# Optimization experiments

Hardware: AMD Instinct MI355X
Metric: run time of the kernel (lower is better)

## Reference

```python
import jax, jax.numpy as jnp
import numpy as np

B, C, CI, H, W = 4, 64, 32, 96, 96  # batch, in_channels, inter_channels, height, width


def conv2d(x, w, b, stride=1, pad=0):
    out = jax.lax.conv_general_dilated(
        x, w, (stride, stride), [(pad, pad), (pad, pad)],
        dimension_numbers=('NCHW', 'OIHW', 'NCHW'))
    return out + b[None, :, None, None]


def maxpool2(x):
    return jax.lax.reduce_window(x, -jnp.inf, jax.lax.max, (1, 1, 2, 2), (1, 1, 2, 2), 'VALID')


def up2(x):
    return jnp.repeat(jnp.repeat(x, 2, axis=2), 2, axis=3)


def bn_train(x, gamma, beta, eps=1e-5):
    # BatchNorm2d in training mode: batch statistics over (N, H, W)
    m = jnp.mean(x, axis=(0, 2, 3), keepdims=True)
    v = jnp.var(x, axis=(0, 2, 3), keepdims=True)
    return gamma[None, :, None, None] * (x - m) * jax.lax.rsqrt(v + eps) + beta[None, :, None, None]


def setup_inputs() -> dict:
    key = jax.random.key(0)
    ks = jax.random.split(key, 20)
    s1 = (2.0 / C) ** 0.5            # kaiming-ish for 1x1 convs
    s3 = (2.0 / (C * 9)) ** 0.5      # kaiming-ish for 3x3 convs
    sw = (2.0 / CI) ** 0.5
    return {
        'x':         jax.random.normal(ks[0], (B, C, H, W), jnp.float32),
        'x_pan':     jax.random.normal(ks[1], (B, C, H, W), jnp.float32),
        'g_w':       jax.random.normal(ks[2], (CI, C, 1, 1), jnp.float32) * s1,
        'g_b':       jnp.zeros((CI,), jnp.float32),
        'g_pan_w':   jax.random.normal(ks[3], (CI, C, 1, 1), jnp.float32) * s1,
        'g_pan_b':   jnp.zeros((CI,), jnp.float32),
        'theta_w':   jax.random.normal(ks[4], (CI, C, 3, 3), jnp.float32) * s3,
        'theta_b':   jax.random.normal(ks[5], (CI,), jnp.float32) * 0.02,
        'phi_w':     jax.random.normal(ks[6], (CI, C, 3, 3), jnp.float32) * s3,
        'phi_b':     jax.random.normal(ks[7], (CI,), jnp.float32) * 0.02,
        'phi_pan_w': jax.random.normal(ks[8], (CI, C, 3, 3), jnp.float32) * s3,
        'phi_pan_b': jax.random.normal(ks[9], (CI,), jnp.float32) * 0.02,
        'W_w':       jax.random.normal(ks[10], (C, CI, 1, 1), jnp.float32) * sw,
        'W_b':       jnp.zeros((C,), jnp.float32),
        'W_gamma':   jnp.ones((C,), jnp.float32),
        'W_beta':    jnp.zeros((C,), jnp.float32),
        'Wp_w':      jax.random.normal(ks[11], (C, CI, 1, 1), jnp.float32) * sw,
        'Wp_b':      jnp.zeros((C,), jnp.float32),
        'Wp_gamma':  jnp.ones((C,), jnp.float32),
        'Wp_beta':   jnp.zeros((C,), jnp.float32),
    }


def reference(x, x_pan, g_w, g_b, g_pan_w, g_pan_b, theta_w, theta_b,
              phi_w, phi_b, phi_pan_w, phi_pan_b,
              W_w, W_b, W_gamma, W_beta, Wp_w, Wp_b, Wp_gamma, Wp_beta):
    b = x.shape[0]
    # self branch
    g_x = maxpool2(conv2d(x, g_w, g_b)).reshape(b, CI, -1)                           # (B,CI,M)
    theta = up2(conv2d(x, theta_w, theta_b, stride=2, pad=1)).reshape(b, CI, -1)     # (B,CI,N)
    phi = up2(maxpool2(conv2d(x, phi_w, phi_b, stride=2, pad=1))).reshape(b, CI, -1) # (B,CI,M)
    f = jnp.einsum('bcn,bcm->bnm', theta, phi)                                       # (B,N,M)
    a = jax.nn.softmax(f, axis=-1)
    y = jnp.einsum('bnm,bcm->bcn', a, g_x).reshape(b, CI, H, W)
    W_y = bn_train(conv2d(y, W_w, W_b), W_gamma, W_beta)
    # cross-modal (pan) branch, sharing theta queries
    g_p = maxpool2(conv2d(x_pan, g_pan_w, g_pan_b)).reshape(b, CI, -1)
    phi_p = up2(maxpool2(conv2d(x_pan, phi_pan_w, phi_pan_b, stride=2, pad=1))).reshape(b, CI, -1)
    f_p = jnp.einsum('bcn,bcm->bnm', theta, phi_p)
    a_p = jax.nn.softmax(f_p, axis=-1)
    y_p = jnp.einsum('bnm,bcm->bcn', a_p, g_p).reshape(b, CI, H, W)
    Wp_y = bn_train(conv2d(y_p, Wp_w, Wp_b), Wp_gamma, Wp_beta)
    return jnp.concatenate([W_y, Wp_y], axis=1)  # (B, 2C, H, W)
```

## Files before the change

### kernel.cpp

```cpp
#include <hip/hip_runtime.h>
#include <math.h>

#define BB   4
#define CIN  64
#define CMID 32
#define HS   96
#define WS   96
#define H2   48
#define W2   48
#define H4   24
#define W4   24
#define N2   (H2*W2)
#define M4   (H4*W4)

__global__ __launch_bounds__(256) void zero_kernel(float* __restrict__ p)
{
    p[threadIdx.x] = 0.f;
}

__global__ __launch_bounds__(128) void conv3x3_kernel(
    const float* __restrict__ x, const float* __restrict__ x_pan,
    const float* __restrict__ theta_w, const float* __restrict__ phi_w,
    const float* __restrict__ phi_pan_w,
    float* __restrict__ Ptheta, float* __restrict__ Pphi)
{
    const int bx = blockIdx.x;
    const int b  = blockIdx.y;
    const int cz = blockIdx.z;

    __shared__ __align__(16) float xs[16][5][104];
    __shared__ float wsm[16][9][32];

    const int tid = threadIdx.x;
    const int c16 = tid & 15;
    const int g   = tid >> 4;

    const float* xin = (cz == 2) ? x_pan : x;
    const float* wgt = (cz == 0) ? theta_w : (cz == 1 ? phi_w : phi_pan_w);

    const int p    = bx >> 1;
    const int half = bx & 1;
    const int row0 = 4*p - 1;

    float acc[2][2][6];
    #pragma unroll
    for (int u = 0; u < 2; ++u)
        #pragma unroll
        for (int o = 0; o < 2; ++o)
            #pragma unroll
            for (int j = 0; j < 6; ++j) acc[u][o][j] = 0.f;

    for (int chunk = 0; chunk < 2; ++chunk) {
        const int ci0 = half*32 + chunk*16;
        __syncthreads();
        for (int u = tid; u < 16*5*26; u += 128) {
            int ci = u / 130, rem = u % 130, rr = rem / 26, k = rem % 26;
            int row = row0 + rr;
            float4 v = {0.f,0.f,0.f,0.f};
            if (row >= 0 && row < HS && k >= 2)
                v = *(const float4*)&xin[((b*CIN + ci0 + ci)*HS + row)*WS + 4*k - 8];
            *(float4*)&xs[ci][rr][4*k] = v;
        }
        for (int u = tid; u < 1152; u += 128) {
            int c2 = u / 36, f = u % 36;
            float4 wv = *(const float4*)&wgt[c2*576 + ci0*9 + 4*f];
            int lin = 4*f;
            wsm[(lin  )/9][(lin  )%9][c2] = wv.x;
            wsm[(lin+1)/9][(lin+1)%9][c2] = wv.y;
            wsm[(lin+2)/9][(lin+2)%9][c2] = wv.z;
            wsm[(lin+3)/9][(lin+3)%9][c2] = wv.w;
        }
        __syncthreads();

        for (int ci = 0; ci < 16; ++ci) {
            float w9a[9], w9b[9];
            #pragma unroll
            for (int kk = 0; kk < 9; ++kk) {
                w9a[kk] = wsm[ci][kk][c16];
                w9b[kk] = wsm[ci][kk][c16 + 16];
            }
            #pragma unroll
            for (int rr = 0; rr < 5; ++rr) {
                const float4* xr = (const float4*)&xs[ci][rr][12*g + 4];
                float4 t0 = xr[0], t1 = xr[1], t2 = xr[2], t3 = xr[3];
                float xv[16] = {t0.x,t0.y,t0.z,t0.w, t1.x,t1.y,t1.z,t1.w,
                                t2.x,t2.y,t2.z,t2.w, t3.x,t3.y,t3.z,t3.w};
                if (rr <= 2) {
                    #pragma unroll
                    for (int j = 0; j < 6; ++j)
                        #pragma unroll
                        for (int kw = 0; kw < 3; ++kw) {
                            float xvv = xv[3 + 2*j + kw];
                            acc[0][0][j] += w9a[rr*3+kw] * xvv;
                            acc[1][0][j] += w9b[rr*3+kw] * xvv;
                        }
                }
                if (rr >= 2) {
                    #pragma unroll
                    for (int j = 0; j < 6; ++j)
                        #pragma unroll
                        for (int kw = 0; kw < 3; ++kw) {
                            float xvv = xv[3 + 2*j + kw];
                            acc[0][1][j] += w9a[(rr-2)*3+kw] * xvv;
                            acc[1][1][j] += w9b[(rr-2)*3+kw] * xvv;
                        }
                }
            }
        }
    }

    if (cz == 0) {
        #pragma unroll
        for (int u = 0; u < 2; ++u)
            #pragma unroll
            for (int o = 0; o < 2; ++o)
                #pragma unroll
                for (int j = 0; j < 6; ++j) {
                    int n = (2*p + o)*48 + 6*g + j;
                    Ptheta[((size_t)(half*4 + b)*N2 + n)*32 + c16 + 16*u] = acc[u][o][j];
                }
    } else {
        const int brn = cz - 1;
        #pragma unroll
        for (int u = 0; u < 2; ++u) {
            float* Pb = Pphi + (size_t)(((half*2 + brn)*4 + b)*32 + c16 + 16*u)*N2;
            #pragma unroll
            for (int o = 0; o < 2; ++o)
                #pragma unroll
                for (int j = 0; j < 6; ++j)
                    Pb[(2*p + o)*48 + 6*g + j] = acc[u][o][j];
        }
    }
}

__global__ __launch_bounds__(256) void phipool_kernel(
    const float* __restrict__ Pphi,
    const float* __restrict__ phi_b, const float* __restrict__ phi_pan_b,
    float* __restrict__ Kp)
{
    const int o = blockIdx.x*256 + threadIdx.x;
    const int br   = o / 73728;
    const int rem  = o % 73728;
    const int b    = rem / 18432;
    const int rem2 = rem % 18432;
    const int co   = rem2 / 576;
    const int k    = rem2 % 576;
    const int pr   = k / 24, pc = k % 24;

    const int h1 = 2*4*32*N2;
    const int base = (((br*4 + b)*32 + co)*48 + 2*pr)*48 + 2*pc;
    float2 a0 = *(const float2*)&Pphi[base];
    float2 a1 = *(const float2*)&Pphi[base + 48];
    float2 c0 = *(const float2*)&Pphi[h1 + base];
    float2 c1 = *(const float2*)&Pphi[h1 + base + 48];
    float v00 = a0.x + c0.x, v01 = a0.y + c0.y;
    float v10 = a1.x + c1.x, v11 = a1.y + c1.y;
    float bv = (br ? phi_pan_b : phi_b)[co];
    Kp[((size_t)(br*4 + b)*576 + k)*32 + co] =
        fmaxf(fmaxf(v00, v01), fmaxf(v10, v11)) + bv;
}

__global__ __launch_bounds__(384) void gconv_kernel(
    const float* __restrict__ x, const float* __restrict__ x_pan,
    const float* __restrict__ g_w, const float* __restrict__ g_b,
    const float* __restrict__ g_pan_w, const float* __restrict__ g_pan_b,
    float* __restrict__ Vv)
{
    const int r4 = blockIdx.x;
    const int ch = blockIdx.y;
    const int bb = blockIdx.z;
    const int br = bb >> 2, b = bb & 3;
    const float* xin = br ? x_pan : x;
    const float* wg  = br ? g_pan_w : g_w;

    __shared__ __align__(16) float xs[32][4][48];
    __shared__ float wl[64*33];
    const int tid = threadIdx.x;
    for (int u = tid; u < 2048; u += 384) {
        int c2 = u >> 6, ci = u & 63;
        wl[ci*33 + c2] = wg[u];
    }

    const int c  = tid & 31;
    const int sl = tid >> 5;
    float4 ac0 = {0,0,0,0}, ac1 = {0,0,0,0}, ac2 = {0,0,0,0}, ac3 = {0,0,0,0};

    for (int ci0 = 0; ci0 < 64; ci0 += 32) {
        __syncthreads();
        for (int u = tid; u < 32*4*12; u += 384) {
            int ci = u / 48, rem = u % 48, r = rem / 12, k = rem % 12;
            *(float4*)&xs[ci][r][4*k] =
                *(const float4*)&xin[((b*64 + ci0 + ci)*96 + 4*r4 + r)*96 + ch*48 + 4*k];
        }
        __syncthreads();
        for (int ci = 0; ci < 32; ++ci) {
            const float wv = wl[(ci0 + ci)*33 + c];
            float4 x0 = *(const float4*)&xs[ci][0][4*sl];
            float4 x1 = *(const float4*)&xs[ci][1][4*sl];
            float4 x2 = *(const float4*)&xs[ci][2][4*sl];
            float4 x3 = *(const float4*)&xs[ci][3][4*sl];
            ac0.x += wv*x0.x; ac0.y += wv*x0.y; ac0.z += wv*x0.z; ac0.w += wv*x0.w;
            ac1.x += wv*x1.x; ac1.y += wv*x1.y; ac1.z += wv*x1.z; ac1.w += wv*x1.w;
            ac2.x += wv*x2.x; ac2.y += wv*x2.y; ac2.z += wv*x2.z; ac2.w += wv*x2.w;
            ac3.x += wv*x3.x; ac3.y += wv*x3.y; ac3.z += wv*x3.z; ac3.w += wv*x3.w;
        }
    }
    float m00 = fmaxf(fmaxf(ac0.x, ac0.y), fmaxf(ac1.x, ac1.y));
    float m01 = fmaxf(fmaxf(ac0.z, ac0.w), fmaxf(ac1.z, ac1.w));
    float m10 = fmaxf(fmaxf(ac2.x, ac2.y), fmaxf(ac3.x, ac3.y));
    float m11 = fmaxf(fmaxf(ac2.z, ac2.w), fmaxf(ac3.z, ac3.w));
    float bv = (br ? g_pan_b : g_b)[c];
    const int k = r4*24 + ch*12 + sl;
    Vv[((size_t)bb*576 + k)*32 + c] = 0.25f*(m00+m01+m10+m11) + bv;
}

__global__ __launch_bounds__(256) void attn_kernel(
    const float* __restrict__ Ptheta, const float* __restrict__ theta_b,
    const float* __restrict__ Kp, const float* __restrict__ Vv,
    const float* __restrict__ W_w, const float* __restrict__ W_b,
    const float* __restrict__ Wp_w, const float* __restrict__ Wp_b,
    float* __restrict__ zbuf, float* __restrict__ Psum, float* __restrict__ Psq)
{
    const int qt = blockIdx.x;
    const int bb = blockIdx.y;
    const int b  = bb & 3;
    const int br = bb >> 2;

    __shared__ float Wl[64*33];
    __shared__ float Wb_s[64];
    __shared__ float mbuf[64];
    __shared__ float zsb[64];
    __shared__ float avbuf[64*33];
    __shared__ float ybuf[16*33];

    const int tid  = threadIdx.x;
    const int ql   = tid & 15;
    const int ks   = tid >> 4;
    const int q    = qt*16 + ql;
    const int lane = tid & 63;
    const int w    = tid >> 6;

    const float* Wsrc = br ? Wp_w : W_w;
    for (int u = tid; u < 2048; u += 256)
        Wl[(u >> 5)*33 + (u & 31)] = Wsrc[u];
    if (tid < 64) Wb_s[tid] = (br ? Wp_b : W_b)[tid];

    float qv[32];
    {
        const float4* P0 = (const float4*)(Ptheta + ((size_t)b*N2 + q)*32);
        const float4* P1 = (const float4*)(Ptheta + ((size_t)(4 + b)*N2 + q)*32);
        const float4* TB = (const float4*)theta_b;
        #pragma unroll
        for (int i = 0; i < 8; ++i) {
            float4 a = P0[i], c = P1[i], t = TB[i];
            qv[4*i]   = a.x + c.x + t.x;
            qv[4*i+1] = a.y + c.y + t.y;
            qv[4*i+2] = a.z + c.z + t.z;
            qv[4*i+3] = a.w + c.w + t.w;
        }
    }

    const float* Kb = Kp + (size_t)bb*576*32;
    const float* Vb = Vv + (size_t)bb*576*32;

    float m = -1e30f;
    for (int jj = 0; jj < 9; ++jj) {
        const int k0 = ks*36 + 4*jj;
        float s[4];
        #pragma unroll
        for (int kk = 0; kk < 4; ++kk) {
            const float4* kr = (const float4*)&Kb[(size_t)(k0 + kk)*32];
            float a0 = 0.f, a1 = 0.f;
            #pragma unroll
            for (int c8 = 0; c8 < 8; ++c8) {
                float4 kv = kr[c8];
                a0 += qv[4*c8]*kv.x + qv[4*c8+2]*kv.z;
                a1 += qv[4*c8+1]*kv.y + qv[4*c8+3]*kv.w;
            }
            s[kk] = a0 + a1;
        }
        m = fmaxf(m, fmaxf(fmaxf(s[0], s[1]), fmaxf(s[2], s[3])));
    }
    m = fmaxf(m, __shfl_xor(m, 16));
    m = fmaxf(m, __shfl_xor(m, 32));
    if (lane < 16) mbuf[w*16 + ql] = m;
    __syncthreads();
    const float M = fmaxf(fmaxf(mbuf[ql], mbuf[16+ql]),
                          fmaxf(mbuf[32+ql], mbuf[48+ql]));

    float av[32];
    #pragma unroll
    for (int c2 = 0; c2 < 32; ++c2) av[c2] = 0.f;
    float z = 0.f;
    for (int jj = 0; jj < 9; ++jj) {
        const int k0 = ks*36 + 4*jj;
        float p[4];
        #pragma unroll
        for (int kk = 0; kk < 4; ++kk) {
            const float4* kr = (const float4*)&Kb[(size_t)(k0 + kk)*32];
            float a0 = 0.f, a1 = 0.f;
            #pragma unroll
            for (int c8 = 0; c8 < 8; ++c8) {
                float4 kv = kr[c8];
                a0 += qv[4*c8]*kv.x + qv[4*c8+2]*kv.z;
                a1 += qv[4*c8+1]*kv.y + qv[4*c8+3]*kv.w;
            }
            p[kk] = __expf(a0 + a1 - M);
            z += p[kk];
        }
        #pragma unroll
        for (int kk = 0; kk < 4; ++kk) {
            const float4* vr = (const float4*)&Vb[(size_t)(k0 + kk)*32];
            #pragma unroll
            for (int c8 = 0; c8 < 8; ++c8) {
                float4 vv = vr[c8];
                av[4*c8]   += p[kk]*vv.x;
                av[4*c8+1] += p[kk]*vv.y;
                av[4*c8+2] += p[kk]*vv.z;
                av[4*c8+3] += p[kk]*vv.w;
            }
        }
    }
    z += __shfl_xor(z, 16); z += __shfl_xor(z, 32);
    #pragma unroll
    for (int c2 = 0; c2 < 32; ++c2) {
        av[c2] += __shfl_xor(av[c2], 16);
        av[c2] += __shfl_xor(av[c2], 32);
    }
    if (lane < 16) {
        #pragma unroll
        for (int c2 = 0; c2 < 32; ++c2) avbuf[(w*16 + ql)*33 + c2] = av[c2];
        zsb[w*16 + ql] = z;
    }
    __syncthreads();

    const float Z = zsb[ql] + zsb[16+ql] + zsb[32+ql] + zsb[48+ql];
    const float inv = 1.0f / Z;
    #pragma unroll
    for (int cc = 0; cc < 2; ++cc) {
        const int c2 = 2*ks + cc;
        float sv = avbuf[ql*33 + c2] + avbuf[(16+ql)*33 + c2]
                 + avbuf[(32+ql)*33 + c2] + avbuf[(48+ql)*33 + c2];
        ybuf[ql*33 + c2] = sv * inv;
    }
    __syncthreads();

    #pragma unroll
    for (int i = 0; i < 4; ++i) {
        const int o  = ks*4 + i;
        const int og = br*64 + o;
        float zv = Wb_s[o];
        #pragma unroll
        for (int c2 = 0; c2 < 32; ++c2)
            zv += Wl[o*33 + c2] * ybuf[ql*33 + c2];
        zbuf[((size_t)og*4 + b)*N2 + q] = zv;
        float s1 = zv, s2 = zv*zv;
        #pragma unroll
        for (int d = 1; d < 16; d <<= 1) {
            s1 += __shfl_xor(s1, d);
            s2 += __shfl_xor(s2, d);
        }
        if (ql == 0) {
            atomicAdd(&Psum[og], s1);
            atomicAdd(&Psq[og],  s2);
        }
    }
}

__global__ __launch_bounds__(576) void bnup_kernel(
    const float* __restrict__ zbuf,
    const float* __restrict__ Psum, const float* __restrict__ Psq,
    const float* __restrict__ W_gamma, const float* __restrict__ W_beta,
    const float* __restrict__ Wp_gamma, const float* __restrict__ Wp_beta,
    float* __restrict__ out)
{
    const int og = blockIdx.x, b = blockIdx.y;
    const int br = og >> 6, o = og & 63;
    const float mean = Psum[og] * (1.0f/9216.0f);
    const float var  = Psq[og] * (1.0f/9216.0f) - mean*mean;
    const float gamma = (br ? Wp_gamma : W_gamma)[o];
    const float beta  = (br ? Wp_beta  : W_beta)[o];
    const float scale = gamma * rsqrtf(var + 1e-5f);
    const float shift = beta - mean*scale;

    const int t = threadIdx.x;
    float4 a = *(const float4*)&zbuf[((size_t)og*4 + b)*N2 + 4*t];
    const int r = t / 12, cs = t % 12;
    float v0 = a.x*scale + shift, v1 = a.y*scale + shift;
    float v2 = a.z*scale + shift, v3 = a.w*scale + shift;
    float4 lo = {v0, v0, v1, v1};
    float4 hi = {v2, v2, v3, v3};
    float* ob = out + ((size_t)(b*128 + og)*96 + 2*r)*96 + 8*cs;
    *(float4*)(ob)       = lo;
    *(float4*)(ob + 4)   = hi;
    *(float4*)(ob + 96)  = lo;
    *(float4*)(ob + 100) = hi;
}

extern "C" void kernel_launch(void* const* d_in, const int* in_sizes, int n_in,
                              void* d_out, int out_size, void* d_ws, size_t ws_size,
                              hipStream_t stream) {
    (void)in_sizes; (void)n_in; (void)out_size; (void)ws_size;
    const float* x         = (const float*)d_in[0];
    const float* x_pan     = (const float*)d_in[1];
    const float* g_w       = (const float*)d_in[2];
    const float* g_b       = (const float*)d_in[3];
    const float* g_pan_w   = (const float*)d_in[4];
    const float* g_pan_b   = (const float*)d_in[5];
    const float* theta_w   = (const float*)d_in[6];
    const float* theta_b   = (const float*)d_in[7];
    const float* phi_w     = (const float*)d_in[8];
    const float* phi_b     = (const float*)d_in[9];
    const float* phi_pan_w = (const float*)d_in[10];
    const float* phi_pan_b = (const float*)d_in[11];
    const float* W_w       = (const float*)d_in[12];
    const float* W_b       = (const float*)d_in[13];
    const float* W_gamma   = (const float*)d_in[14];
    const float* W_beta    = (const float*)d_in[15];
    const float* Wp_w      = (const float*)d_in[16];
    const float* Wp_b      = (const float*)d_in[17];
    const float* Wp_gamma  = (const float*)d_in[18];
    const float* Wp_beta   = (const float*)d_in[19];

    float* out = (float*)d_out;
    float* ws  = (float*)d_ws;

    float* Ptheta = ws;
    float* Pphi   = Ptheta + 589824;
    float* zbuf   = Pphi;
    float* Kp     = Pphi + 1179648;
    float* Vv     = Kp + 147456;
    float* Psum   = Vv + 147456;
    float* Psq    = Psum + 128;

    zero_kernel<<<dim3(1), 256, 0, stream>>>(Psum);
    conv3x3_kernel<<<dim3(48, 4, 3), 128, 0, stream>>>(
        x, x_pan, theta_w, phi_w, phi_pan_w, Ptheta, Pphi);
    phipool_kernel<<<dim3(576), 256, 0, stream>>>(Pphi, phi_b, phi_pan_b, Kp);
    gconv_kernel<<<dim3(24, 2, 8), 384, 0, stream>>>(
        x, x_pan, g_w, g_b, g_pan_w, g_pan_b, Vv);
    attn_kernel<<<dim3(144, 8), 256, 0, stream>>>(
        Ptheta, theta_b, Kp, Vv, W_w, W_b, Wp_w, Wp_b, zbuf, Psum, Psq);
    bnup_kernel<<<dim3(128, 4), 576, 0, stream>>>(
        zbuf, Psum, Psq, W_gamma, W_beta, Wp_gamma, Wp_beta, out);
}
```

Measured before the change: 441.1 us.

## Restructure attention to materialize scores in LDS and drop atomic BN stats

The attention kernel now has one thread per key (576 threads). Each thread computes scores for 16 queries and writes them to shared memory, then runs the softmax over those rows and a P·V pass that reads a transposed V layout. This replaces the old two-pass recomputation of QK scores, where each thread also held 32 accumulators. BatchNorm statistics are now written as per-block partial sums and reduced inside bnup, which removes the global atomics and the zero kernel. The conv3x3 channel chunk is halved to shrink LDS use, at the cost of more sync rounds.

```diff
diff --git a/kernel.cpp b/kernel.cpp
--- a/kernel.cpp
+++ b/kernel.cpp
@@ -13,11 +13,6 @@
 #define N2   (H2*W2)
 #define M4   (H4*W4)
 
-__global__ __launch_bounds__(256) void zero_kernel(float* __restrict__ p)
-{
-    p[threadIdx.x] = 0.f;
-}
-
 __global__ __launch_bounds__(128) void conv3x3_kernel(
     const float* __restrict__ x, const float* __restrict__ x_pan,
     const float* __restrict__ theta_w, const float* __restrict__ phi_w,
@@ -28,8 +23,8 @@
     const int b  = blockIdx.y;
     const int cz = blockIdx.z;
 
-    __shared__ __align__(16) float xs[16][5][104];
-    __shared__ float wsm[16][9][32];
+    __shared__ __align__(16) float xs[8][5][104];
+    __shared__ float wsm[8][9][32];
 
     const int tid = threadIdx.x;
     const int c16 = tid & 15;
@@ -50,10 +45,10 @@
             #pragma unroll
             for (int j = 0; j < 6; ++j) acc[u][o][j] = 0.f;
 
-    for (int chunk = 0; chunk < 2; ++chunk) {
-        const int ci0 = half*32 + chunk*16;
+    for (int chunk = 0; chunk < 4; ++chunk) {
+        const int ci0 = half*32 + chunk*8;
         __syncthreads();
-        for (int u = tid; u < 16*5*26; u += 128) {
+        for (int u = tid; u < 8*5*26; u += 128) {
             int ci = u / 130, rem = u % 130, rr = rem / 26, k = rem % 26;
             int row = row0 + rr;
             float4 v = {0.f,0.f,0.f,0.f};
@@ -61,8 +56,8 @@
                 v = *(const float4*)&xin[((b*CIN + ci0 + ci)*HS + row)*WS + 4*k - 8];
             *(float4*)&xs[ci][rr][4*k] = v;
         }
-        for (int u = tid; u < 1152; u += 128) {
-            int c2 = u / 36, f = u % 36;
+        for (int u = tid; u < 576; u += 128) {
+            int c2 = u / 18, f = u % 18;
             float4 wv = *(const float4*)&wgt[c2*576 + ci0*9 + 4*f];
             int lin = 4*f;
             wsm[(lin  )/9][(lin  )%9][c2] = wv.x;
@@ -72,7 +67,7 @@
         }
         __syncthreads();
 
-        for (int ci = 0; ci < 16; ++ci) {
+        for (int ci = 0; ci < 8; ++ci) {
             float w9a[9], w9b[9];
             #pragma unroll
             for (int kk = 0; kk < 9; ++kk) {
@@ -164,7 +159,7 @@
     const float* __restrict__ x, const float* __restrict__ x_pan,
     const float* __restrict__ g_w, const float* __restrict__ g_b,
     const float* __restrict__ g_pan_w, const float* __restrict__ g_pan_b,
-    float* __restrict__ Vv)
+    float* __restrict__ Vt)
 {
     const int r4 = blockIdx.x;
     const int ch = blockIdx.y;
@@ -211,179 +206,181 @@
     float m11 = fmaxf(fmaxf(ac2.z, ac2.w), fmaxf(ac3.z, ac3.w));
     float bv = (br ? g_pan_b : g_b)[c];
     const int k = r4*24 + ch*12 + sl;
-    Vv[((size_t)bb*576 + k)*32 + c] = 0.25f*(m00+m01+m10+m11) + bv;
-}
-
-__global__ __launch_bounds__(256) void attn_kernel(
+    Vt[((size_t)bb*32 + c)*576 + k] = 0.25f*(m00+m01+m10+m11) + bv;
+}
+
+__global__ __launch_bounds__(576, 5) void attn_kernel(
     const float* __restrict__ Ptheta, const float* __restrict__ theta_b,
-    const float* __restrict__ Kp, const float* __restrict__ Vv,
+    const float* __restrict__ Kp, const float* __restrict__ Vt,
     const float* __restrict__ W_w, const float* __restrict__ W_b,
     const float* __restrict__ Wp_w, const float* __restrict__ Wp_b,
-    float* __restrict__ zbuf, float* __restrict__ Psum, float* __restrict__ Psq)
+    float* __restrict__ zbuf, float* __restrict__ Pp1, float* __restrict__ Pp2)
 {
     const int qt = blockIdx.x;
     const int bb = blockIdx.y;
     const int b  = bb & 3;
     const int br = bb >> 2;
-
-    __shared__ float Wl[64*33];
-    __shared__ float Wb_s[64];
-    __shared__ float mbuf[64];
-    __shared__ float zsb[64];
-    __shared__ float avbuf[64*33];
-    __shared__ float ybuf[16*33];
-
-    const int tid  = threadIdx.x;
-    const int ql   = tid & 15;
-    const int ks   = tid >> 4;
-    const int q    = qt*16 + ql;
-    const int lane = tid & 63;
-    const int w    = tid >> 6;
-
+    const int q0 = qt*16;
+
+    __shared__ __align__(16) float Pt[16*580];
+    __shared__ __align__(16) float Qs[16*36];
+    __shared__ float ybuf[16*36];
+    __shared__ float Wt[32*64];
+    __shared__ float zinv[16];
+    __shared__ float s1b[512], s2b[512];
+
+    const int tid = threadIdx.x;
+
+    if (tid < 512) {
+        const int q = tid >> 5, c = tid & 31;
+        Qs[q*36 + c] = Ptheta[((size_t)b*N2 + q0 + q)*32 + c]
+                     + Ptheta[((size_t)(4 + b)*N2 + q0 + q)*32 + c]
+                     + theta_b[c];
+    }
     const float* Wsrc = br ? Wp_w : W_w;
-    for (int u = tid; u < 2048; u += 256)
-        Wl[(u >> 5)*33 + (u & 31)] = Wsrc[u];
-    if (tid < 64) Wb_s[tid] = (br ? Wp_b : W_b)[tid];
-
-    float qv[32];
+    for (int u = tid; u < 2048; u += 576) {
+        const int o = u >> 5, c = u & 31;
+        Wt[c*64 + o] = Wsrc[u];
+    }
+    __syncthreads();
+
     {
-        const float4* P0 = (const float4*)(Ptheta + ((size_t)b*N2 + q)*32);
-        const float4* P1 = (const float4*)(Ptheta + ((size_t)(4 + b)*N2 + q)*32);
-        const float4* TB = (const float4*)theta_b;
-        #pragma unroll
-        for (int i = 0; i < 8; ++i) {
-            float4 a = P0[i], c = P1[i], t = TB[i];
-            qv[4*i]   = a.x + c.x + t.x;
-            qv[4*i+1] = a.y + c.y + t.y;
-            qv[4*i+2] = a.z + c.z + t.z;
-            qv[4*i+3] = a.w + c.w + t.w;
-        }
-    }
-
-    const float* Kb = Kp + (size_t)bb*576*32;
-    const float* Vb = Vv + (size_t)bb*576*32;
-
-    float m = -1e30f;
-    for (int jj = 0; jj < 9; ++jj) {
-        const int k0 = ks*36 + 4*jj;
-        float s[4];
-        #pragma unroll
-        for (int kk = 0; kk < 4; ++kk) {
-            const float4* kr = (const float4*)&Kb[(size_t)(k0 + kk)*32];
-            float a0 = 0.f, a1 = 0.f;
-            #pragma unroll
-            for (int c8 = 0; c8 < 8; ++c8) {
-                float4 kv = kr[c8];
-                a0 += qv[4*c8]*kv.x + qv[4*c8+2]*kv.z;
-                a1 += qv[4*c8+1]*kv.y + qv[4*c8+3]*kv.w;
+        const float* krow = Kp + ((size_t)bb*576 + tid)*32;
+        float4 kf[8];
+        #pragma unroll
+        for (int i = 0; i < 8; ++i) kf[i] = ((const float4*)krow)[i];
+        float s[16];
+        #pragma unroll
+        for (int q = 0; q < 16; ++q) {
+            const float4* qr = (const float4*)&Qs[q*36];
+            float a0 = 0.f, a1 = 0.f, a2 = 0.f, a3 = 0.f;
+            #pragma unroll
+            for (int i = 0; i < 8; ++i) {
+                float4 qf = qr[i];
+                a0 += qf.x*kf[i].x; a1 += qf.y*kf[i].y;
+                a2 += qf.z*kf[i].z; a3 += qf.w*kf[i].w;
             }
-            s[kk] = a0 + a1;
-        }
-        m = fmaxf(m, fmaxf(fmaxf(s[0], s[1]), fmaxf(s[2], s[3])));
-    }
-    m = fmaxf(m, __shfl_xor(m, 16));
-    m = fmaxf(m, __shfl_xor(m, 32));
-    if (lane < 16) mbuf[w*16 + ql] = m;
-    __syncthreads();
-    const float M = fmaxf(fmaxf(mbuf[ql], mbuf[16+ql]),
-                          fmaxf(mbuf[32+ql], mbuf[48+ql]));
-
-    float av[32];
-    #pragma unroll
-    for (int c2 = 0; c2 < 32; ++c2) av[c2] = 0.f;
-    float z = 0.f;
-    for (int jj = 0; jj < 9; ++jj) {
-        const int k0 = ks*36 + 4*jj;
-        float p[4];
-        #pragma unroll
-        for (int kk = 0; kk < 4; ++kk) {
-            const float4* kr = (const float4*)&Kb[(size_t)(k0 + kk)*32];
-            float a0 = 0.f, a1 = 0.f;
-            #pragma unroll
-            for (int c8 = 0; c8 < 8; ++c8) {
-                float4 kv = kr[c8];
-                a0 += qv[4*c8]*kv.x + qv[4*c8+2]*kv.z;
-                a1 += qv[4*c8+1]*kv.y + qv[4*c8+3]*kv.w;
-            }
-            p[kk] = __expf(a0 + a1 - M);
-            z += p[kk];
-        }
-        #pragma unroll
-        for (int kk = 0; kk < 4; ++kk) {
-            const float4* vr = (const float4*)&Vb[(size_t)(k0 + kk)*32];
-            #pragma unroll
-            for (int c8 = 0; c8 < 8; ++c8) {
-                float4 vv = vr[c8];
-                av[4*c8]   += p[kk]*vv.x;
-                av[4*c8+1] += p[kk]*vv.y;
-                av[4*c8+2] += p[kk]*vv.z;
-                av[4*c8+3] += p[kk]*vv.w;
-            }
-        }
-    }
-    z += __shfl_xor(z, 16); z += __shfl_xor(z, 32);
-    #pragma unroll
-    for (int c2 = 0; c2 < 32; ++c2) {
-        av[c2] += __shfl_xor(av[c2], 16);
-        av[c2] += __shfl_xor(av[c2], 32);
-    }
-    if (lane < 16) {
-        #pragma unroll
-        for (int c2 = 0; c2 < 32; ++c2) avbuf[(w*16 + ql)*33 + c2] = av[c2];
-        zsb[w*16 + ql] = z;
-    }
-    __syncthreads();
-
-    const float Z = zsb[ql] + zsb[16+ql] + zsb[32+ql] + zsb[48+ql];
-    const float inv = 1.0f / Z;
-    #pragma unroll
-    for (int cc = 0; cc < 2; ++cc) {
-        const int c2 = 2*ks + cc;
-        float sv = avbuf[ql*33 + c2] + avbuf[(16+ql)*33 + c2]
-                 + avbuf[(32+ql)*33 + c2] + avbuf[(48+ql)*33 + c2];
-        ybuf[ql*33 + c2] = sv * inv;
-    }
-    __syncthreads();
-
-    #pragma unroll
-    for (int i = 0; i < 4; ++i) {
-        const int o  = ks*4 + i;
-        const int og = br*64 + o;
-        float zv = Wb_s[o];
-        #pragma unroll
-        for (int c2 = 0; c2 < 32; ++c2)
-            zv += Wl[o*33 + c2] * ybuf[ql*33 + c2];
-        zbuf[((size_t)og*4 + b)*N2 + q] = zv;
-        float s1 = zv, s2 = zv*zv;
-        #pragma unroll
-        for (int d = 1; d < 16; d <<= 1) {
-            s1 += __shfl_xor(s1, d);
-            s2 += __shfl_xor(s2, d);
-        }
-        if (ql == 0) {
-            atomicAdd(&Psum[og], s1);
-            atomicAdd(&Psq[og],  s2);
-        }
+            s[q] = (a0 + a1) + (a2 + a3);
+        }
+        #pragma unroll
+        for (int q = 0; q < 16; ++q) Pt[q*580 + tid] = s[q];
+    }
+    __syncthreads();
+
+    if (tid < 256) {
+        const int q = tid >> 4, sl = tid & 15;
+        float* row = &Pt[q*580 + 36*sl];
+        float4 f[9];
+        #pragma unroll
+        for (int j = 0; j < 9; ++j) f[j] = *(const float4*)&row[4*j];
+        float m = -1e30f;
+        #pragma unroll
+        for (int j = 0; j < 9; ++j)
+            m = fmaxf(m, fmaxf(fmaxf(f[j].x, f[j].y), fmaxf(f[j].z, f[j].w)));
+        m = fmaxf(m, __shfl_xor(m, 1));
+        m = fmaxf(m, __shfl_xor(m, 2));
+        m = fmaxf(m, __shfl_xor(m, 4));
+        m = fmaxf(m, __shfl_xor(m, 8));
+        float z = 0.f;
+        #pragma unroll
+        for (int j = 0; j < 9; ++j) {
+            f[j].x = __expf(f[j].x - m); f[j].y = __expf(f[j].y - m);
+            f[j].z = __expf(f[j].z - m); f[j].w = __expf(f[j].w - m);
+            z += (f[j].x + f[j].y) + (f[j].z + f[j].w);
+            *(float4*)&row[4*j] = f[j];
+        }
+        z += __shfl_xor(z, 1); z += __shfl_xor(z, 2);
+        z += __shfl_xor(z, 4); z += __shfl_xor(z, 8);
+        if (sl == 0) zinv[q] = 1.0f / z;
+    }
+    __syncthreads();
+
+    if (tid < 512) {
+        const int q = tid >> 5, c = tid & 31;
+        const float* vrow = Vt + ((size_t)bb*32 + c)*576;
+        const float* prow = &Pt[q*580];
+        float a0 = 0.f, a1 = 0.f, a2 = 0.f, a3 = 0.f;
+        #pragma unroll 4
+        for (int kk = 0; kk < 144; ++kk) {
+            float4 pa = *(const float4*)&prow[4*kk];
+            float4 va = *(const float4*)&vrow[4*kk];
+            a0 += pa.x*va.x; a1 += pa.y*va.y;
+            a2 += pa.z*va.z; a3 += pa.w*va.w;
+        }
+        ybuf[q*36 + c] = ((a0 + a1) + (a2 + a3)) * zinv[q];
+    }
+    __syncthreads();
+
+    if (tid < 512) {
+        const int q = tid >> 5, o2 = tid & 31;
+        const float* Wbias = br ? Wp_b : W_b;
+        float z0a = 0.f, z0b = 0.f, z1a = 0.f, z1b = 0.f;
+        #pragma unroll
+        for (int c2 = 0; c2 < 32; c2 += 2) {
+            float y0 = ybuf[q*36 + c2], y1 = ybuf[q*36 + c2 + 1];
+            z0a += Wt[c2*64 + o2]*y0;        z0b += Wt[(c2+1)*64 + o2]*y1;
+            z1a += Wt[c2*64 + o2 + 32]*y0;   z1b += Wt[(c2+1)*64 + o2 + 32]*y1;
+        }
+        float z0 = Wbias[o2]      + z0a + z0b;
+        float z1 = Wbias[o2 + 32] + z1a + z1b;
+        const int n = q0 + q;
+        zbuf[((size_t)(br*64 + o2)*4 + b)*N2 + n]      = z0;
+        zbuf[((size_t)(br*64 + o2 + 32)*4 + b)*N2 + n] = z1;
+        float t0 = z0 + __shfl_xor(z0, 32);
+        float t1 = z1 + __shfl_xor(z1, 32);
+        float u0 = z0*z0; u0 += __shfl_xor(u0, 32);
+        float u1 = z1*z1; u1 += __shfl_xor(u1, 32);
+        if ((tid & 32) == 0) {
+            const int w = tid >> 6;
+            s1b[w*64 + o2]      = t0;  s1b[w*64 + o2 + 32] = t1;
+            s2b[w*64 + o2]      = u0;  s2b[w*64 + o2 + 32] = u1;
+        }
+    }
+    __syncthreads();
+    if (tid < 64) {
+        float ps = 0.f, pq = 0.f;
+        #pragma unroll
+        for (int w = 0; w < 8; ++w) { ps += s1b[w*64 + tid]; pq += s2b[w*64 + tid]; }
+        Pp1[(size_t)(br*64 + tid)*576 + b*144 + qt] = ps;
+        Pp2[(size_t)(br*64 + tid)*576 + b*144 + qt] = pq;
     }
 }
 
 __global__ __launch_bounds__(576) void bnup_kernel(
     const float* __restrict__ zbuf,
-    const float* __restrict__ Psum, const float* __restrict__ Psq,
+    const float* __restrict__ Pp1, const float* __restrict__ Pp2,
     const float* __restrict__ W_gamma, const float* __restrict__ W_beta,
     const float* __restrict__ Wp_gamma, const float* __restrict__ Wp_beta,
     float* __restrict__ out)
 {
     const int og = blockIdx.x, b = blockIdx.y;
     const int br = og >> 6, o = og & 63;
-    const float mean = Psum[og] * (1.0f/9216.0f);
-    const float var  = Psq[og] * (1.0f/9216.0f) - mean*mean;
-    const float gamma = (br ? Wp_gamma : W_gamma)[o];
-    const float beta  = (br ? Wp_beta  : W_beta)[o];
-    const float scale = gamma * rsqrtf(var + 1e-5f);
-    const float shift = beta - mean*scale;
-
     const int t = threadIdx.x;
+
+    __shared__ float sb1[9], sb2[9], bc[2];
+    float ps = Pp1[(size_t)og*576 + t];
+    float pq = Pp2[(size_t)og*576 + t];
+    #pragma unroll
+    for (int d = 1; d < 64; d <<= 1) {
+        ps += __shfl_xor(ps, d);
+        pq += __shfl_xor(pq, d);
+    }
+    if ((t & 63) == 0) { sb1[t >> 6] = ps; sb2[t >> 6] = pq; }
+    __syncthreads();
+    if (t == 0) {
+        float s = 0.f, qq = 0.f;
+        #pragma unroll
+        for (int w = 0; w < 9; ++w) { s += sb1[w]; qq += sb2[w]; }
+        const float mean = s * (1.0f/9216.0f);
+        const float var  = qq * (1.0f/9216.0f) - mean*mean;
+        const float gamma = (br ? Wp_gamma : W_gamma)[o];
+        const float beta  = (br ? Wp_beta  : W_beta)[o];
+        const float scale = gamma * rsqrtf(var + 1e-5f);
+        bc[0] = scale; bc[1] = beta - mean*scale;
+    }
+    __syncthreads();
+    const float scale = bc[0], shift = bc[1];
+
     float4 a = *(const float4*)&zbuf[((size_t)og*4 + b)*N2 + 4*t];
     const int r = t / 12, cs = t % 12;
     float v0 = a.x*scale + shift, v1 = a.y*scale + shift;
@@ -429,18 +426,17 @@
     float* Pphi   = Ptheta + 589824;
     float* zbuf   = Pphi;
     float* Kp     = Pphi + 1179648;
-    float* Vv     = Kp + 147456;
-    float* Psum   = Vv + 147456;
-    float* Psq    = Psum + 128;
-
-    zero_kernel<<<dim3(1), 256, 0, stream>>>(Psum);
+    float* Vt     = Kp + 147456;
+    float* Pp1    = Vt + 147456;
+    float* Pp2    = Pp1 + 73728;
+
     conv3x3_kernel<<<dim3(48, 4, 3), 128, 0, stream>>>(
         x, x_pan, theta_w, phi_w, phi_pan_w, Ptheta, Pphi);
     phipool_kernel<<<dim3(576), 256, 0, stream>>>(Pphi, phi_b, phi_pan_b, Kp);
     gconv_kernel<<<dim3(24, 2, 8), 384, 0, stream>>>(
-        x, x_pan, g_w, g_b, g_pan_w, g_pan_b, Vv);
-    attn_kernel<<<dim3(144, 8), 256, 0, stream>>>(
-        Ptheta, theta_b, Kp, Vv, W_w, W_b, Wp_w, Wp_b, zbuf, Psum, Psq);
+        x, x_pan, g_w, g_b, g_pan_w, g_pan_b, Vt);
+    attn_kernel<<<dim3(144, 8), 576, 0, stream>>>(
+        Ptheta, theta_b, Kp, Vt, W_w, W_b, Wp_w, Wp_b, zbuf, Pp1, Pp2);
     bnup_kernel<<<dim3(128, 4), 576, 0, stream>>>(
-        zbuf, Psum, Psq, W_gamma, W_beta, Wp_gamma, Wp_beta, out);
-}
+        zbuf, Pp1, Pp2, W_gamma, W_beta, Wp_gamma, Wp_beta, out);
+}
```

Measured after the change: 444.6 us. About the same (+0.8%).
